# Optimization experiments

Hardware: AMD Instinct MI355X
Metric: run time of the kernel (lower is better)

## Reference

```python
import jax, jax.numpy as jnp
import numpy as np
from jax import lax

# GlobalSeed with a standard Mamba2 (SSD) core.
# C=64 feature channels, G=8 token dim, d_inner=16, d_state=16, nheads=2, headdim=8, d_conv=3.
C_FEAT, G, D_INNER, D_STATE, NHEADS, HEADDIM, D_CONV = 64, 8, 16, 16, 2, 8, 3
CONV_DIM = D_INNER + 2 * D_STATE  # 48
D_IN_PROJ = 2 * D_INNER + 2 * D_STATE + NHEADS  # 66


def setup_inputs() -> dict:
    key = jax.random.key(0)
    ks = jax.random.split(key, 16)
    B, H, W = 16, 128, 128
    s = 0.02
    return {
        "x": jax.random.normal(ks[0], (B, C_FEAT, H, W), jnp.float32),
        "tok_w": s * jax.random.normal(ks[1], (G, C_FEAT), jnp.float32),
        "tok_b": jnp.zeros((G,), jnp.float32),
        "detok_w": s * jax.random.normal(ks[2], (C_FEAT, G), jnp.float32),
        "detok_b": jnp.zeros((C_FEAT,), jnp.float32),
        "in_proj_w": s * jax.random.normal(ks[3], (D_IN_PROJ, G), jnp.float32),
        "in_proj_b": jnp.zeros((D_IN_PROJ,), jnp.float32),
        "conv_w": s * jax.random.normal(ks[4], (CONV_DIM, D_CONV), jnp.float32),
        "conv_b": jnp.zeros((CONV_DIM,), jnp.float32),
        "A_log": jnp.log(jnp.arange(1, NHEADS + 1, dtype=jnp.float32)),
        "D": jnp.ones((NHEADS,), jnp.float32),
        "dt_bias": 0.1 * jax.random.normal(ks[5], (NHEADS,), jnp.float32),
        "norm_w": jnp.ones((D_INNER,), jnp.float32),
        "out_w": s * jax.random.normal(ks[6], (G, D_INNER), jnp.float32),
        "out_b": jnp.zeros((G,), jnp.float32),
    }


def _mamba2(gt, in_proj_w, in_proj_b, conv_w, conv_b, A_log, D, dt_bias, norm_w, out_w, out_b):
    # gt: (B, L, G) tokens
    B, L, _ = gt.shape
    zxbcdt = gt @ in_proj_w.T + in_proj_b  # (B, L, 66)
    z = zxbcdt[..., :D_INNER]
    xBC = zxbcdt[..., D_INNER:D_INNER + CONV_DIM]
    dt = zxbcdt[..., D_INNER + CONV_DIM:]  # (B, L, nheads)
    # depthwise causal conv1d over L
    xBC = lax.conv_general_dilated(
        xBC.transpose(0, 2, 1), conv_w[:, None, :], (1,), [(D_CONV - 1, 0)],
        feature_group_count=CONV_DIM).transpose(0, 2, 1) + conv_b
    xBC = jax.nn.silu(xBC)
    xr = xBC[..., :D_INNER].reshape(B, L, NHEADS, HEADDIM)
    Bm = xBC[..., D_INNER:D_INNER + D_STATE]   # (B, L, N)
    Cm = xBC[..., D_INNER + D_STATE:]          # (B, L, N)
    dt = jax.nn.softplus(dt + dt_bias)          # (B, L, H)
    dec = jnp.exp(dt * (-jnp.exp(A_log)))       # (B, L, H)

    def step(h, inp):
        xt, Bt, Ct, dtt, dct = inp  # (B,H,P) (B,N) (B,N) (B,H) (B,H)
        h = dct[:, :, None, None] * h + (dtt[:, :, None] * xt)[..., None] * Bt[:, None, None, :]
        y = jnp.einsum('bhpn,bn->bhp', h, Ct)
        return h, y

    h0 = jnp.zeros((B, NHEADS, HEADDIM, D_STATE), gt.dtype)
    xs = (xr.transpose(1, 0, 2, 3), Bm.transpose(1, 0, 2), Cm.transpose(1, 0, 2),
          dt.transpose(1, 0, 2), dec.transpose(1, 0, 2))
    _, ys = lax.scan(step, h0, xs)  # (L, B, H, P)
    y = ys.transpose(1, 0, 2, 3) + D[None, None, :, None] * xr
    y = y.reshape(B, L, D_INNER)
    y = y * jax.nn.silu(z)  # gated
    y = y * lax.rsqrt(jnp.mean(y * y, axis=-1, keepdims=True) + 1e-5) * norm_w  # RMSNormGated
    return y @ out_w.T + out_b  # (B, L, G)


def reference(x, tok_w, tok_b, detok_w, detok_b, in_proj_w, in_proj_b, conv_w, conv_b,
              A_log, D, dt_bias, norm_w, out_w, out_b):
    B, C, H, W = x.shape
    L = H * W
    g = jnp.einsum('bchw,gc->bghw', x, tok_w) + tok_b[None, :, None, None]
    gt = g.reshape(B, G, L).transpose(0, 2, 1)  # (B, L, G)
    gt = _mamba2(gt, in_proj_w, in_proj_b, conv_w, conv_b, A_log, D, dt_bias, norm_w, out_w, out_b) + gt
    g2 = gt.transpose(0, 2, 1).reshape(B, G, H, W)
    return x + jnp.einsum('bghw,cg->bchw', g2, detok_w) + detok_b[None, :, None, None]
```

## Files before the change

kernel.cpp:

```cpp
#include <hip/hip_runtime.h>
#include <math.h>

#define NB 16
#define CF 64
#define LL 16384
#define GG 8
#define NH 2
#define SEG 64
#define NSEG 256
#define GRP 16
#define NGRP 16
#define CHK 16
#define NCHKS 4

static constexpr size_t OFF_GT = 0;
static constexpr size_t OFF_C  = OFF_GT + (size_t)NB*LL*GG;
static constexpr size_t OFF_YL = OFF_C  + (size_t)NB*LL*16;
static constexpr size_t OFF_CA = OFF_YL + (size_t)NB*LL*16;
static constexpr size_t OFF_PH = OFF_CA + (size_t)NB*LL*NH;
static constexpr size_t OFF_CP = OFF_PH + (size_t)NB*NSEG*256;
static constexpr size_t OFF_U2 = OFF_CP + (size_t)NB*NSEG*NH;
static constexpr size_t OFF_AG = OFF_U2 + (size_t)NB*NGRP*256;
static constexpr size_t OFF_GH = OFF_AG + (size_t)NB*NGRP*NH;
static constexpr size_t OFF_G2 = OFF_GH + (size_t)NB*NGRP*256;
static constexpr size_t WS_FLOATS = OFF_G2 + (size_t)NB*LL*GG;

__device__ __forceinline__ float siluf(float v){ return v / (1.f + __expf(-v)); }
__device__ __forceinline__ float softplusf(float v){ return v > 20.f ? v : log1pf(__expf(v)); }

__device__ __forceinline__ void load8(float* d, const float* p){
    float4 a = ((const float4*)p)[0];
    float4 b = ((const float4*)p)[1];
    d[0]=a.x; d[1]=a.y; d[2]=a.z; d[3]=a.w;
    d[4]=b.x; d[5]=b.y; d[6]=b.z; d[7]=b.w;
}
__device__ __forceinline__ void load16(float* d, const float* p){
    load8(d, p); load8(d+8, p+8);
}

__global__ __launch_bounds__(256) void k1a_tok(
    const float* __restrict__ x, const float* __restrict__ tok_w,
    const float* __restrict__ tok_b, float* __restrict__ gtw)
{
    __shared__ float s_tok[GG*CF];
    int tid = threadIdx.x;
    int b  = blockIdx.x >> 4;
    int ck = blockIdx.x & 15;
    int l0 = (ck << 10) + (tid << 2);
    for (int i = tid; i < GG*CF; i += 256) s_tok[i] = tok_w[i];
    __syncthreads();
    float acc[4][GG];
    #pragma unroll
    for (int r = 0; r < 4; ++r)
        #pragma unroll
        for (int g = 0; g < GG; ++g) acc[r][g] = tok_b[g];
    const float* xb = x + (size_t)b*CF*LL + l0;
    #pragma unroll 8
    for (int c = 0; c < CF; ++c) {
        float4 xv = *(const float4*)(xb + (size_t)c*LL);
        float xa[4] = {xv.x, xv.y, xv.z, xv.w};
        #pragma unroll
        for (int g = 0; g < GG; ++g) {
            float w = s_tok[g*CF + c];
            #pragma unroll
            for (int r = 0; r < 4; ++r) acc[r][g] = fmaf(xa[r], w, acc[r][g]);
        }
    }
    float* gp = gtw + ((size_t)b*LL + l0)*GG;
    #pragma unroll
    for (int r = 0; r < 4; ++r) {
        ((float4*)gp)[r*2+0] = make_float4(acc[r][0],acc[r][1],acc[r][2],acc[r][3]);
        ((float4*)gp)[r*2+1] = make_float4(acc[r][4],acc[r][5],acc[r][6],acc[r][7]);
    }
}

__global__ __launch_bounds__(256, 1) void k2_fused(
    const float* __restrict__ gtw,
    const float* __restrict__ ipw, const float* __restrict__ ipb,
    const float* __restrict__ cw, const float* __restrict__ cb,
    const float* __restrict__ A_log, const float* __restrict__ dt_bias,
    const float* __restrict__ Dv,
    float* __restrict__ cmw, float* __restrict__ ylw, float* __restrict__ caw,
    float* __restrict__ phw, float* __restrict__ cpw,
    float* __restrict__ U2w, float* __restrict__ Agw)
{
    __shared__ float s_x [16][17][20];
    __shared__ float s_B [16][17][20];
    __shared__ float s_Ct[16][17][20];
    __shared__ float s_dt[16][17][2], s_de[16][17][2], s_ca[16][17][2];
    __shared__ float s_U[16][2][8][17];
    __shared__ float s_cAs[16][2];
    __shared__ float s_ipw[48*8];
    __shared__ float s_ipb2[48], s_cw2[144], s_cb2[48], s_wdt[16];

    int tid = threadIdx.x;
    int b = blockIdx.x >> 4, grp = blockIdx.x & 15;
    for (int i = tid; i < 384; i += 256) s_ipw[i] = ipw[128 + i];
    if (tid < 48) { s_ipb2[tid] = ipb[16 + tid]; s_cb2[tid] = cb[tid]; }
    else if (tid >= 64 && tid < 208) s_cw2[tid - 64] = cw[tid - 64];
    else if (tid >= 224 && tid < 240) s_wdt[tid - 224] = ipw[512 + (tid - 224)];
    __syncthreads();

    int sj = tid >> 4, tl = tid & 15;
    int he = (tid >> 3) & 1, p = tid & 7;
    int hp = he * 8 + p;
    int eb = he * 128 + p * 16;
    float a0e = __expf(A_log[0]), a1e = __expf(A_log[1]);
    float dtb0 = dt_bias[0], dtb1 = dt_bias[1];
    float bdt0 = ipb[64], bdt1 = ipb[65];
    float D_he = Dv[he];
    float h[16];
    #pragma unroll
    for (int n = 0; n < 16; ++n) h[n] = 0.f;
    float cA = 1.f;
    int lb = grp * 1024 + sj * 64;

    for (int c = 0; c < NCHKS; ++c) {
        int l = lb + c * CHK + tl;
        size_t gb = ((size_t)b * LL + l) * GG;
        float g0[8], g1[8], g2v[8];
        #pragma unroll
        for (int g = 0; g < 8; ++g) { g1[g] = 0.f; g2v[g] = 0.f; }
        load8(g0, gtw + gb);
        if (l >= 1) load8(g1, gtw + gb - GG);
        if (l >= 2) load8(g2v, gtw + gb - 2*GG);
        float vals[48];
        #pragma unroll
        for (int ch = 0; ch < 48; ++ch) {
            float4 w0 = *(const float4*)&s_ipw[ch*8];
            float4 w1 = *(const float4*)&s_ipw[ch*8+4];
            float wv[8] = {w0.x,w0.y,w0.z,w0.w,w1.x,w1.y,w1.z,w1.w};
            float bia = s_ipb2[ch];
            float tA = bia, tB = bia, tC = bia;
            #pragma unroll
            for (int g = 0; g < 8; ++g) {
                tA = fmaf(g0[g],  wv[g], tA);
                tB = fmaf(g1[g],  wv[g], tB);
                tC = fmaf(g2v[g], wv[g], tC);
            }
            if (l < 1) tB = 0.f;
            if (l < 2) tC = 0.f;
            float a = s_cb2[ch];
            a = fmaf(tC, s_cw2[ch*3+0], a);
            a = fmaf(tB, s_cw2[ch*3+1], a);
            a = fmaf(tA, s_cw2[ch*3+2], a);
            vals[ch] = siluf(a);
        }
        #pragma unroll
        for (int q = 0; q < 4; ++q) {
            int ph_ = ((q + tl) & 3) * 4;
            *(float4*)&s_x [sj][tl][ph_] = make_float4(vals[q*4+0],vals[q*4+1],vals[q*4+2],vals[q*4+3]);
            *(float4*)&s_B [sj][tl][ph_] = make_float4(vals[16+q*4+0],vals[16+q*4+1],vals[16+q*4+2],vals[16+q*4+3]);
            *(float4*)&s_Ct[sj][tl][ph_] = make_float4(vals[32+q*4+0],vals[32+q*4+1],vals[32+q*4+2],vals[32+q*4+3]);
        }
        {
            size_t pb = (size_t)b * LL + l;
            float4* cp4 = (float4*)(cmw + pb*16);
            #pragma unroll
            for (int q = 0; q < 4; ++q)
                cp4[q] = make_float4(vals[32+q*4+0],vals[32+q*4+1],vals[32+q*4+2],vals[32+q*4+3]);
        }
        {
            float d0 = bdt0, d1 = bdt1;
            #pragma unroll
            for (int g = 0; g < 8; ++g) {
                d0 = fmaf(g0[g], s_wdt[g],   d0);
                d1 = fmaf(g0[g], s_wdt[8+g], d1);
            }
            float dt0 = softplusf(d0 + dtb0), dt1 = softplusf(d1 + dtb1);
            *(float2*)&s_dt[sj][tl][0] = make_float2(dt0, dt1);
            *(float2*)&s_de[sj][tl][0] = make_float2(__expf(-dt0*a0e), __expf(-dt1*a1e));
        }
        __syncthreads();
        for (int t = 0; t < CHK; ++t) {
            float a   = s_de[sj][t][he];
            float dtv = s_dt[sj][t][he];
            float xv  = s_x[sj][t][(((hp>>2)+t)&3)*4 + (hp&3)];
            float u = dtv * xv;
            float Bv[16], Cv[16];
            #pragma unroll
            for (int q = 0; q < 4; ++q) {
                float4 bq = *(const float4*)&s_B [sj][t][((q+t)&3)*4];
                float4 cq = *(const float4*)&s_Ct[sj][t][((q+t)&3)*4];
                Bv[q*4+0]=bq.x; Bv[q*4+1]=bq.y; Bv[q*4+2]=bq.z; Bv[q*4+3]=bq.w;
                Cv[q*4+0]=cq.x; Cv[q*4+1]=cq.y; Cv[q*4+2]=cq.z; Cv[q*4+3]=cq.w;
            }
            float y = 0.f;
            #pragma unroll
            for (int n = 0; n < 16; ++n) {
                h[n] = fmaf(a, h[n], u * Bv[n]);
                y = fmaf(h[n], Cv[n], y);
            }
            cA *= a;
            s_x[sj][t][(((hp>>2)+t)&3)*4 + (hp&3)] = fmaf(D_he, xv, y);
            if (p == 0) s_ca[sj][t][he] = cA;
        }
        __syncthreads();
        {
            size_t pb = (size_t)b * LL + l;
            float4* yp4 = (float4*)(ylw + pb*16);
            #pragma unroll
            for (int q = 0; q < 4; ++q)
                yp4[q] = *(const float4*)&s_x[sj][tl][((q+tl)&3)*4];
            *(float2*)(caw + pb*2) = *(const float2*)&s_ca[sj][tl][0];
        }
        __syncthreads();
    }

    #pragma unroll
    for (int n = 0; n < 16; ++n) s_U[sj][he][p][n] = h[n];
    if (p == 0) s_cAs[sj][he] = cA;
    __syncthreads();
    float hin[16];
    #pragma unroll
    for (int n = 0; n < 16; ++n) hin[n] = 0.f;
    float cp = 1.f;
    for (int j = 0; j < GRP-1; ++j) {
        if (j < sj) {
            float Aj = s_cAs[j][he];
            #pragma unroll
            for (int n = 0; n < 16; ++n) hin[n] = fmaf(Aj, hin[n], s_U[j][he][p][n]);
            cp *= Aj;
        }
    }
    int seg = grp * GRP + sj;
    {
        float* php = phw + (((size_t)b*NSEG + seg) << 8) + eb;
        #pragma unroll
        for (int q = 0; q < 4; ++q)
            ((float4*)php)[q] = make_float4(hin[q*4+0],hin[q*4+1],hin[q*4+2],hin[q*4+3]);
        if (p == 0) cpw[((size_t)b*NSEG + seg)*2 + he] = cp;
    }
    if (sj == GRP-1) {
        float A15 = s_cAs[15][he];
        float* u2p = U2w + (((size_t)b*NGRP + grp) << 8) + eb;
        #pragma unroll
        for (int q = 0; q < 4; ++q) {
            float4 v4;
            v4.x = fmaf(A15, hin[q*4+0], h[q*4+0]);
            v4.y = fmaf(A15, hin[q*4+1], h[q*4+1]);
            v4.z = fmaf(A15, hin[q*4+2], h[q*4+2]);
            v4.w = fmaf(A15, hin[q*4+3], h[q*4+3]);
            ((float4*)u2p)[q] = v4;
        }
        if (p == 0) Agw[((size_t)b*NGRP + grp)*2 + he] = cp * A15;
    }
}

__global__ void k4b_grp(const float* __restrict__ U2w, const float* __restrict__ Agw,
                        float* __restrict__ ghw)
{
    int b = blockIdx.x, e = threadIdx.x, he = e >> 7;
    float u[NGRP], ag[NGRP];
    #pragma unroll
    for (int g = 0; g < NGRP; ++g) {
        u[g]  = U2w[(((size_t)b*NGRP + g) << 8) + e];
        ag[g] = Agw[((size_t)b*NGRP + g)*2 + he];
    }
    float h = 0.f;
    #pragma unroll
    for (int g = 0; g < NGRP; ++g) {
        ghw[(((size_t)b*NGRP + g) << 8) + e] = h;
        h = fmaf(ag[g], h, u[g]);
    }
}

__global__ __launch_bounds__(256, 4) void k5a_epi(
    const float* __restrict__ gtw, const float* __restrict__ cmw,
    const float* __restrict__ ylw, const float* __restrict__ caw,
    const float* __restrict__ phw, const float* __restrict__ cpw,
    const float* __restrict__ ghw,
    const float* __restrict__ ipw, const float* __restrict__ ipb,
    const float* __restrict__ norm_w,
    const float* __restrict__ out_w, const float* __restrict__ out_b,
    float* __restrict__ g2w)
{
    __shared__ float s_hin[4][256];
    __shared__ float s_zw[16*GG], s_ow[GG*16];
    int tid = threadIdx.x;
    int b  = blockIdx.x >> 6;
    int ck = blockIdx.x & 63;
    int grp = ck >> 2;
    float gh = ghw[(((size_t)b*NGRP + grp) << 8) + tid];
    #pragma unroll
    for (int k = 0; k < 4; ++k) {
        int seg = ck*4 + k;
        float cpv = cpw[((size_t)b*NSEG + seg)*2 + (tid >> 7)];
        s_hin[k][tid] = fmaf(cpv, gh, phw[(((size_t)b*NSEG + seg) << 8) + tid]);
    }
    if (tid < 128) s_zw[tid] = ipw[tid];
    else s_ow[tid-128] = out_w[tid-128];
    __syncthreads();
    size_t pb = (size_t)b*LL + (ck<<8) + tid;
    int sub = tid >> 6;
    float gv[8]; load8(gv, gtw + pb*GG);
    float Cv[16], ylv[16];
    load16(Cv,  cmw + pb*16);
    load16(ylv, ylw + pb*16);
    float2 ca = *(const float2*)(caw + pb*2);
    float vv[16], ss = 0.f;
    #pragma unroll
    for (int hp = 0; hp < 16; ++hp) {
        float dot = 0.f;
        #pragma unroll
        for (int nn = 0; nn < 16; ++nn)
            dot = fmaf(Cv[nn], s_hin[sub][(hp>>3)*128 + (hp&7)*16 + nn], dot);
        float zz = ipb[hp];
        #pragma unroll
        for (int g = 0; g < GG; ++g) zz = fmaf(gv[g], s_zw[hp*GG+g], zz);
        float y = fmaf((hp>>3) ? ca.y : ca.x, dot, ylv[hp]);
        float w = y * siluf(zz);
        vv[hp] = w; ss = fmaf(w, w, ss);
    }
    float rn = rsqrtf(ss*(1.f/16.f) + 1e-5f);
    float o[8];
    #pragma unroll
    for (int g = 0; g < GG; ++g) o[g] = out_b[g] + gv[g];
    #pragma unroll
    for (int hp = 0; hp < 16; ++hp) {
        float wv = vv[hp] * rn * norm_w[hp];
        #pragma unroll
        for (int g = 0; g < GG; ++g) o[g] = fmaf(wv, s_ow[g*16+hp], o[g]);
    }
    float* gp = g2w + pb*GG;
    ((float4*)gp)[0] = make_float4(o[0],o[1],o[2],o[3]);
    ((float4*)gp)[1] = make_float4(o[4],o[5],o[6],o[7]);
}

__global__ __launch_bounds__(256, 4) void k5b_detok(
    const float* __restrict__ x, const float* __restrict__ g2w,
    const float* __restrict__ dkw, const float* __restrict__ dkb,
    float* __restrict__ outp)
{
    __shared__ float s_dw[CF*GG];
    __shared__ float s_db[CF];
    int tid = threadIdx.x;
    int b  = blockIdx.x >> 4;
    int ck = blockIdx.x & 15;
    int l0 = (ck << 10) + (tid << 2);
    for (int i = tid; i < CF*GG; i += 256) s_dw[i] = dkw[i];
    if (tid < CF) s_db[tid] = dkb[tid];
    __syncthreads();
    float g2v[4][8];
    const float* gp = g2w + ((size_t)b*LL + l0)*GG;
    #pragma unroll
    for (int r = 0; r < 4; ++r) load8(g2v[r], gp + r*GG);
    const float* xb = x + (size_t)b*CF*LL + l0;
    float* ob = outp + (size_t)b*CF*LL + l0;
    #pragma unroll 4
    for (int c = 0; c < CF; ++c) {
        float4 xv = *(const float4*)(xb + (size_t)c*LL);
        float bias = s_db[c];
        float oa[4] = {xv.x+bias, xv.y+bias, xv.z+bias, xv.w+bias};
        #pragma unroll
        for (int g = 0; g < GG; ++g) {
            float w = s_dw[c*GG+g];
            #pragma unroll
            for (int r = 0; r < 4; ++r) oa[r] = fmaf(g2v[r][g], w, oa[r]);
        }
        *(float4*)(ob + (size_t)c*LL) = make_float4(oa[0],oa[1],oa[2],oa[3]);
    }
}

extern "C" void kernel_launch(void* const* d_in, const int* in_sizes, int n_in,
                              void* d_out, int out_size, void* d_ws, size_t ws_size,
                              hipStream_t stream) {
    const float* x       = (const float*)d_in[0];
    const float* tok_w   = (const float*)d_in[1];
    const float* tok_b   = (const float*)d_in[2];
    const float* detok_w = (const float*)d_in[3];
    const float* detok_b = (const float*)d_in[4];
    const float* ipw     = (const float*)d_in[5];
    const float* ipb     = (const float*)d_in[6];
    const float* cw      = (const float*)d_in[7];
    const float* cb      = (const float*)d_in[8];
    const float* A_log   = (const float*)d_in[9];
    const float* Dv      = (const float*)d_in[10];
    const float* dt_bias = (const float*)d_in[11];
    const float* norm_w  = (const float*)d_in[12];
    const float* out_w   = (const float*)d_in[13];
    const float* out_b   = (const float*)d_in[14];
    float* ws = (float*)d_ws;
    float* outp = (float*)d_out;

    if (ws_size < WS_FLOATS * sizeof(float)) return;

    k1a_tok<<<NB*16, 256, 0, stream>>>(x, tok_w, tok_b, ws+OFF_GT);
    k2_fused<<<NB*NGRP, 256, 0, stream>>>(ws+OFF_GT, ipw, ipb, cw, cb,
        A_log, dt_bias, Dv, ws+OFF_C, ws+OFF_YL, ws+OFF_CA,
        ws+OFF_PH, ws+OFF_CP, ws+OFF_U2, ws+OFF_AG);
    k4b_grp<<<NB, 256, 0, stream>>>(ws+OFF_U2, ws+OFF_AG, ws+OFF_GH);
    k5a_epi<<<NB*64, 256, 0, stream>>>(ws+OFF_GT, ws+OFF_C, ws+OFF_YL, ws+OFF_CA,
        ws+OFF_PH, ws+OFF_CP, ws+OFF_GH, ipw, ipb, norm_w, out_w, out_b, ws+OFF_G2);
    k5b_detok<<<NB*16, 256, 0, stream>>>(x, ws+OFF_G2, detok_w, detok_b, outp);
}
```

Measured before the change: 114.8 us.

## Halve scan segment length, double blocks, and software-pipeline the SSD recurrence

Result: faster. 110.1 us (-4.1%).

```diff
diff --git a/kernel.cpp b/kernel.cpp
--- a/kernel.cpp
+++ b/kernel.cpp
@@ -6,12 +6,12 @@
 #define LL 16384
 #define GG 8
 #define NH 2
-#define SEG 64
-#define NSEG 256
+#define SEG 32
+#define NSEG 512
 #define GRP 16
-#define NGRP 16
+#define NGRP 32
 #define CHK 16
-#define NCHKS 4
+#define NCHKS 2
 
 static constexpr size_t OFF_GT = 0;
 static constexpr size_t OFF_C  = OFF_GT + (size_t)NB*LL*GG;
@@ -74,7 +74,7 @@
     }
 }
 
-__global__ __launch_bounds__(256, 1) void k2_fused(
+__global__ __launch_bounds__(256, 2) void k2_fused(
     const float* __restrict__ gtw,
     const float* __restrict__ ipw, const float* __restrict__ ipb,
     const float* __restrict__ cw, const float* __restrict__ cb,
@@ -87,14 +87,13 @@
     __shared__ float s_x [16][17][20];
     __shared__ float s_B [16][17][20];
     __shared__ float s_Ct[16][17][20];
-    __shared__ float s_dt[16][17][2], s_de[16][17][2], s_ca[16][17][2];
-    __shared__ float s_U[16][2][8][17];
+    __shared__ float s_dt[16][16][2], s_de[16][16][2], s_ca[16][16][2];
     __shared__ float s_cAs[16][2];
     __shared__ float s_ipw[48*8];
     __shared__ float s_ipb2[48], s_cw2[144], s_cb2[48], s_wdt[16];
 
     int tid = threadIdx.x;
-    int b = blockIdx.x >> 4, grp = blockIdx.x & 15;
+    int b = blockIdx.x >> 5, grp = blockIdx.x & 31;
     for (int i = tid; i < 384; i += 256) s_ipw[i] = ipw[128 + i];
     if (tid < 48) { s_ipb2[tid] = ipb[16 + tid]; s_cb2[tid] = cb[tid]; }
     else if (tid >= 64 && tid < 208) s_cw2[tid - 64] = cw[tid - 64];
@@ -113,17 +112,21 @@
     #pragma unroll
     for (int n = 0; n < 16; ++n) h[n] = 0.f;
     float cA = 1.f;
-    int lb = grp * 1024 + sj * 64;
-
-    for (int c = 0; c < NCHKS; ++c) {
-        int l = lb + c * CHK + tl;
+    int lb = grp * (GRP*SEG) + sj * SEG;
+
+    float g0[8], g1[8], g2v[8];
+    {
+        int l = lb + tl;
         size_t gb = ((size_t)b * LL + l) * GG;
-        float g0[8], g1[8], g2v[8];
         #pragma unroll
         for (int g = 0; g < 8; ++g) { g1[g] = 0.f; g2v[g] = 0.f; }
         load8(g0, gtw + gb);
         if (l >= 1) load8(g1, gtw + gb - GG);
         if (l >= 2) load8(g2v, gtw + gb - 2*GG);
+    }
+
+    for (int c = 0; c < NCHKS; ++c) {
+        int l = lb + c * CHK + tl;
         float vals[48];
         #pragma unroll
         for (int ch = 0; ch < 48; ++ch) {
@@ -171,29 +174,59 @@
             *(float2*)&s_dt[sj][tl][0] = make_float2(dt0, dt1);
             *(float2*)&s_de[sj][tl][0] = make_float2(__expf(-dt0*a0e), __expf(-dt1*a1e));
         }
+        if (c + 1 < NCHKS) {
+            int l2 = lb + (c+1) * CHK + tl;
+            size_t gb2 = ((size_t)b * LL + l2) * GG;
+            load8(g0,  gtw + gb2);
+            load8(g1,  gtw + gb2 - GG);
+            load8(g2v, gtw + gb2 - 2*GG);
+        }
         __syncthreads();
-        for (int t = 0; t < CHK; ++t) {
-            float a   = s_de[sj][t][he];
-            float dtv = s_dt[sj][t][he];
-            float xv  = s_x[sj][t][(((hp>>2)+t)&3)*4 + (hp&3)];
-            float u = dtv * xv;
-            float Bv[16], Cv[16];
+        {
+            float a_c  = s_de[sj][0][he];
+            float dt_c = s_dt[sj][0][he];
+            float x_c  = s_x[sj][0][(((hp>>2))&3)*4 + (hp&3)];
+            float4 bq[4], cq[4];
             #pragma unroll
             for (int q = 0; q < 4; ++q) {
-                float4 bq = *(const float4*)&s_B [sj][t][((q+t)&3)*4];
-                float4 cq = *(const float4*)&s_Ct[sj][t][((q+t)&3)*4];
-                Bv[q*4+0]=bq.x; Bv[q*4+1]=bq.y; Bv[q*4+2]=bq.z; Bv[q*4+3]=bq.w;
-                Cv[q*4+0]=cq.x; Cv[q*4+1]=cq.y; Cv[q*4+2]=cq.z; Cv[q*4+3]=cq.w;
+                bq[q] = *(const float4*)&s_B [sj][0][(q&3)*4];
+                cq[q] = *(const float4*)&s_Ct[sj][0][(q&3)*4];
             }
-            float y = 0.f;
-            #pragma unroll
-            for (int n = 0; n < 16; ++n) {
-                h[n] = fmaf(a, h[n], u * Bv[n]);
-                y = fmaf(h[n], Cv[n], y);
+            #pragma unroll
+            for (int t = 0; t < CHK; ++t) {
+                float a = a_c, dtv = dt_c, xv = x_c;
+                float4 nb[4], nc[4];
+                float na = 0.f, ndt = 0.f, nx = 0.f;
+                if (t + 1 < CHK) {
+                    na  = s_de[sj][t+1][he];
+                    ndt = s_dt[sj][t+1][he];
+                    nx  = s_x[sj][t+1][(((hp>>2)+t+1)&3)*4 + (hp&3)];
+                    #pragma unroll
+                    for (int q = 0; q < 4; ++q) {
+                        nb[q] = *(const float4*)&s_B [sj][t+1][((q+t+1)&3)*4];
+                        nc[q] = *(const float4*)&s_Ct[sj][t+1][((q+t+1)&3)*4];
+                    }
+                }
+                float u = dtv * xv;
+                float Bv[16], Cv[16];
+                #pragma unroll
+                for (int q = 0; q < 4; ++q) {
+                    Bv[q*4+0]=bq[q].x; Bv[q*4+1]=bq[q].y; Bv[q*4+2]=bq[q].z; Bv[q*4+3]=bq[q].w;
+                    Cv[q*4+0]=cq[q].x; Cv[q*4+1]=cq[q].y; Cv[q*4+2]=cq[q].z; Cv[q*4+3]=cq[q].w;
+                }
+                float y = 0.f;
+                #pragma unroll
+                for (int n = 0; n < 16; ++n) {
+                    h[n] = fmaf(a, h[n], u * Bv[n]);
+                    y = fmaf(h[n], Cv[n], y);
+                }
+                cA *= a;
+                s_x[sj][t][(((hp>>2)+t)&3)*4 + (hp&3)] = fmaf(D_he, xv, y);
+                if (p == 0) s_ca[sj][t][he] = cA;
+                a_c = na; dt_c = ndt; x_c = nx;
+                #pragma unroll
+                for (int q = 0; q < 4; ++q) { bq[q] = nb[q]; cq[q] = nc[q]; }
             }
-            cA *= a;
-            s_x[sj][t][(((hp>>2)+t)&3)*4 + (hp&3)] = fmaf(D_he, xv, y);
-            if (p == 0) s_ca[sj][t][he] = cA;
         }
         __syncthreads();
         {
@@ -207,6 +240,7 @@
         __syncthreads();
     }
 
+    float (*s_U)[2][8][17] = reinterpret_cast<float(*)[2][8][17]>(&s_x[0][0][0]);
     #pragma unroll
     for (int n = 0; n < 16; ++n) s_U[sj][he][p][n] = h[n];
     if (p == 0) s_cAs[sj][he] = cA;
@@ -275,16 +309,16 @@
     const float* __restrict__ out_w, const float* __restrict__ out_b,
     float* __restrict__ g2w)
 {
-    __shared__ float s_hin[4][256];
+    __shared__ float s_hin[8][256];
     __shared__ float s_zw[16*GG], s_ow[GG*16];
     int tid = threadIdx.x;
     int b  = blockIdx.x >> 6;
     int ck = blockIdx.x & 63;
-    int grp = ck >> 2;
+    int grp = ck >> 1;
     float gh = ghw[(((size_t)b*NGRP + grp) << 8) + tid];
     #pragma unroll
-    for (int k = 0; k < 4; ++k) {
-        int seg = ck*4 + k;
+    for (int k = 0; k < 8; ++k) {
+        int seg = ck*8 + k;
         float cpv = cpw[((size_t)b*NSEG + seg)*2 + (tid >> 7)];
         s_hin[k][tid] = fmaf(cpv, gh, phw[(((size_t)b*NSEG + seg) << 8) + tid]);
     }
@@ -292,7 +326,7 @@
     else s_ow[tid-128] = out_w[tid-128];
     __syncthreads();
     size_t pb = (size_t)b*LL + (ck<<8) + tid;
-    int sub = tid >> 6;
+    int sub = tid >> 5;
     float gv[8]; load8(gv, gtw + pb*GG);
     float Cv[16], ylv[16];
     load16(Cv,  cmw + pb*16);
```

## Replace sequential intra-chunk SSM scan with chunked SSD matmul form

Applied to the files above, without the earlier changes.

Result: slower. 144.7 us (+26.0%).

```diff
diff --git a/kernel.cpp b/kernel.cpp
--- a/kernel.cpp
+++ b/kernel.cpp
@@ -6,21 +6,20 @@
 #define LL 16384
 #define GG 8
 #define NH 2
-#define SEG 64
-#define NSEG 256
-#define GRP 16
+#define CHN 64
+#define NCH 256
 #define NGRP 16
-#define CHK 16
-#define NCHKS 4
 
 static constexpr size_t OFF_GT = 0;
 static constexpr size_t OFF_C  = OFF_GT + (size_t)NB*LL*GG;
 static constexpr size_t OFF_YL = OFF_C  + (size_t)NB*LL*16;
 static constexpr size_t OFF_CA = OFF_YL + (size_t)NB*LL*16;
-static constexpr size_t OFF_PH = OFF_CA + (size_t)NB*LL*NH;
-static constexpr size_t OFF_CP = OFF_PH + (size_t)NB*NSEG*256;
-static constexpr size_t OFF_U2 = OFF_CP + (size_t)NB*NSEG*NH;
-static constexpr size_t OFF_AG = OFF_U2 + (size_t)NB*NGRP*256;
+static constexpr size_t OFF_U2 = OFF_CA + (size_t)NB*LL*NH;
+static constexpr size_t OFF_AC = OFF_U2 + (size_t)NB*NCH*256;
+static constexpr size_t OFF_PH = OFF_AC + (size_t)NB*NCH*NH;
+static constexpr size_t OFF_CP = OFF_PH + (size_t)NB*NCH*256;
+static constexpr size_t OFF_UG = OFF_CP + (size_t)NB*NCH*NH;
+static constexpr size_t OFF_AG = OFF_UG + (size_t)NB*NGRP*256;
 static constexpr size_t OFF_GH = OFF_AG + (size_t)NB*NGRP*NH;
 static constexpr size_t OFF_G2 = OFF_GH + (size_t)NB*NGRP*256;
 static constexpr size_t WS_FLOATS = OFF_G2 + (size_t)NB*LL*GG;
@@ -74,69 +73,56 @@
     }
 }
 
-__global__ __launch_bounds__(256, 1) void k2_fused(
+__global__ __launch_bounds__(256, 4) void k2_ssd(
     const float* __restrict__ gtw,
     const float* __restrict__ ipw, const float* __restrict__ ipb,
     const float* __restrict__ cw, const float* __restrict__ cb,
     const float* __restrict__ A_log, const float* __restrict__ dt_bias,
     const float* __restrict__ Dv,
     float* __restrict__ cmw, float* __restrict__ ylw, float* __restrict__ caw,
-    float* __restrict__ phw, float* __restrict__ cpw,
-    float* __restrict__ U2w, float* __restrict__ Agw)
-{
-    __shared__ float s_x [16][17][20];
-    __shared__ float s_B [16][17][20];
-    __shared__ float s_Ct[16][17][20];
-    __shared__ float s_dt[16][17][2], s_de[16][17][2], s_ca[16][17][2];
-    __shared__ float s_U[16][2][8][17];
-    __shared__ float s_cAs[16][2];
-    __shared__ float s_ipw[48*8];
-    __shared__ float s_ipb2[48], s_cw2[144], s_cb2[48], s_wdt[16];
+    float* __restrict__ U2w, float* __restrict__ Acw)
+{
+    __shared__ float s_x [64][20];
+    __shared__ float s_Ct[64][17];
+    __shared__ float s_BT[16][68];
+    __shared__ float s_G [64][68];
+    __shared__ float s_dt[64][2], s_nda[64][2], s_la[64][2], s_w[64][2];
+    __shared__ float s_ipw[48*8], s_ipb2[48], s_cw2[144], s_cb2[48], s_wdt[16];
 
     int tid = threadIdx.x;
-    int b = blockIdx.x >> 4, grp = blockIdx.x & 15;
+    int b = blockIdx.x >> 8, c = blockIdx.x & 255;
     for (int i = tid; i < 384; i += 256) s_ipw[i] = ipw[128 + i];
     if (tid < 48) { s_ipb2[tid] = ipb[16 + tid]; s_cb2[tid] = cb[tid]; }
     else if (tid >= 64 && tid < 208) s_cw2[tid - 64] = cw[tid - 64];
     else if (tid >= 224 && tid < 240) s_wdt[tid - 224] = ipw[512 + (tid - 224)];
     __syncthreads();
 
-    int sj = tid >> 4, tl = tid & 15;
-    int he = (tid >> 3) & 1, p = tid & 7;
-    int hp = he * 8 + p;
-    int eb = he * 128 + p * 16;
     float a0e = __expf(A_log[0]), a1e = __expf(A_log[1]);
     float dtb0 = dt_bias[0], dtb1 = dt_bias[1];
     float bdt0 = ipb[64], bdt1 = ipb[65];
-    float D_he = Dv[he];
-    float h[16];
-    #pragma unroll
-    for (int n = 0; n < 16; ++n) h[n] = 0.f;
-    float cA = 1.f;
-    int lb = grp * 1024 + sj * 64;
-
-    for (int c = 0; c < NCHKS; ++c) {
-        int l = lb + c * CHK + tl;
-        size_t gb = ((size_t)b * LL + l) * GG;
+    float D0 = Dv[0], D1 = Dv[1];
+
+    {
+        int r = tid >> 2, sub = tid & 3;
+        int l = c*CHN + r;
+        size_t gb = ((size_t)b*LL + l)*GG;
         float g0[8], g1[8], g2v[8];
         #pragma unroll
         for (int g = 0; g < 8; ++g) { g1[g] = 0.f; g2v[g] = 0.f; }
         load8(g0, gtw + gb);
         if (l >= 1) load8(g1, gtw + gb - GG);
         if (l >= 2) load8(g2v, gtw + gb - 2*GG);
-        float vals[48];
-        #pragma unroll
-        for (int ch = 0; ch < 48; ++ch) {
-            float4 w0 = *(const float4*)&s_ipw[ch*8];
-            float4 w1 = *(const float4*)&s_ipw[ch*8+4];
-            float wv[8] = {w0.x,w0.y,w0.z,w0.w,w1.x,w1.y,w1.z,w1.w};
+        #pragma unroll
+        for (int k = 0; k < 12; ++k) {
+            int ch = sub*12 + k;
             float bia = s_ipb2[ch];
             float tA = bia, tB = bia, tC = bia;
             #pragma unroll
             for (int g = 0; g < 8; ++g) {
-                tA = fmaf(g0[g],  wv[g], tA);
-                tB = fmaf(g1[g],  wv[g], tB);
-                tC = fmaf(g2v[g], wv[g], tC);
+                float wv = s_ipw[ch*8+g];
+                tA = fmaf(g0[g],  wv, tA);
+                tB = fmaf(g1[g],  wv, tB);
+                tC = fmaf(g2v[g], wv, tC);
             }
             if (l < 1) tB = 0.f;
             if (l < 2) tC = 0.f;
@@ -144,23 +130,12 @@
             a = fmaf(tC, s_cw2[ch*3+0], a);
             a = fmaf(tB, s_cw2[ch*3+1], a);
             a = fmaf(tA, s_cw2[ch*3+2], a);
-            vals[ch] = siluf(a);
-        }
-        #pragma unroll
-        for (int q = 0; q < 4; ++q) {
-            int ph_ = ((q + tl) & 3) * 4;
-            *(float4*)&s_x [sj][tl][ph_] = make_float4(vals[q*4+0],vals[q*4+1],vals[q*4+2],vals[q*4+3]);
-            *(float4*)&s_B [sj][tl][ph_] = make_float4(vals[16+q*4+0],vals[16+q*4+1],vals[16+q*4+2],vals[16+q*4+3]);
-            *(float4*)&s_Ct[sj][tl][ph_] = make_float4(vals[32+q*4+0],vals[32+q*4+1],vals[32+q*4+2],vals[32+q*4+3]);
-        }
-        {
-            size_t pb = (size_t)b * LL + l;
-            float4* cp4 = (float4*)(cmw + pb*16);
-            #pragma unroll
-            for (int q = 0; q < 4; ++q)
-                cp4[q] = make_float4(vals[32+q*4+0],vals[32+q*4+1],vals[32+q*4+2],vals[32+q*4+3]);
-        }
-        {
+            float v = siluf(a);
+            if (ch < 16)      s_x[r][ch] = v;
+            else if (ch < 32) s_BT[ch-16][r] = v;
+            else              s_Ct[r][ch-32] = v;
+        }
+        if (sub == 0) {
             float d0 = bdt0, d1 = bdt1;
             #pragma unroll
             for (int g = 0; g < 8; ++g) {
@@ -168,100 +143,122 @@
                 d1 = fmaf(g0[g], s_wdt[8+g], d1);
             }
             float dt0 = softplusf(d0 + dtb0), dt1 = softplusf(d1 + dtb1);
-            *(float2*)&s_dt[sj][tl][0] = make_float2(dt0, dt1);
-            *(float2*)&s_de[sj][tl][0] = make_float2(__expf(-dt0*a0e), __expf(-dt1*a1e));
-        }
-        __syncthreads();
-        for (int t = 0; t < CHK; ++t) {
-            float a   = s_de[sj][t][he];
-            float dtv = s_dt[sj][t][he];
-            float xv  = s_x[sj][t][(((hp>>2)+t)&3)*4 + (hp&3)];
-            float u = dtv * xv;
-            float Bv[16], Cv[16];
-            #pragma unroll
-            for (int q = 0; q < 4; ++q) {
-                float4 bq = *(const float4*)&s_B [sj][t][((q+t)&3)*4];
-                float4 cq = *(const float4*)&s_Ct[sj][t][((q+t)&3)*4];
-                Bv[q*4+0]=bq.x; Bv[q*4+1]=bq.y; Bv[q*4+2]=bq.z; Bv[q*4+3]=bq.w;
-                Cv[q*4+0]=cq.x; Cv[q*4+1]=cq.y; Cv[q*4+2]=cq.z; Cv[q*4+3]=cq.w;
+            s_dt[r][0] = dt0; s_dt[r][1] = dt1;
+            s_nda[r][0] = -dt0*a0e; s_nda[r][1] = -dt1*a1e;
+        }
+    }
+    __syncthreads();
+    {
+        int rr = tid >> 2, q = tid & 3;
+        float4 cv = make_float4(s_Ct[rr][q*4+0], s_Ct[rr][q*4+1],
+                                s_Ct[rr][q*4+2], s_Ct[rr][q*4+3]);
+        ((float4*)(cmw + ((size_t)b*LL + c*CHN + rr)*16))[q] = cv;
+    }
+    if (tid < 64) {
+        int rr = tid;
+        float v0 = s_nda[rr][0], v1 = s_nda[rr][1];
+        #pragma unroll
+        for (int off = 1; off < 64; off <<= 1) {
+            float t0 = __shfl_up(v0, off);
+            float t1 = __shfl_up(v1, off);
+            if (rr >= off) { v0 += t0; v1 += t1; }
+        }
+        s_la[rr][0] = v0; s_la[rr][1] = v1;
+        *(float2*)(caw + ((size_t)b*LL + c*CHN + rr)*2) =
+            make_float2(__expf(v0), __expf(v1));
+        float f0 = __shfl(v0, 63), f1 = __shfl(v1, 63);
+        s_w[rr][0] = __expf(f0 - v0) * s_dt[rr][0];
+        s_w[rr][1] = __expf(f1 - v1) * s_dt[rr][1];
+        if (rr == 63)
+            *(float2*)(Acw + ((size_t)b*NCH + c)*2) = make_float2(__expf(f0), __expf(f1));
+    }
+    __syncthreads();
+    {
+        int t0 = (tid >> 4) * 4, s0 = (tid & 15) * 4;
+        float acc[4][4];
+        #pragma unroll
+        for (int i = 0; i < 4; ++i)
+            #pragma unroll
+            for (int j = 0; j < 4; ++j) acc[i][j] = 0.f;
+        #pragma unroll
+        for (int n = 0; n < 16; ++n) {
+            float c0 = s_Ct[t0+0][n], c1 = s_Ct[t0+1][n];
+            float c2 = s_Ct[t0+2][n], c3 = s_Ct[t0+3][n];
+            float4 bb = *(const float4*)&s_BT[n][s0];
+            float bv[4] = {bb.x, bb.y, bb.z, bb.w};
+            #pragma unroll
+            for (int j = 0; j < 4; ++j) {
+                acc[0][j] = fmaf(c0, bv[j], acc[0][j]);
+                acc[1][j] = fmaf(c1, bv[j], acc[1][j]);
+                acc[2][j] = fmaf(c2, bv[j], acc[2][j]);
+                acc[3][j] = fmaf(c3, bv[j], acc[3][j]);
             }
-            float y = 0.f;
-            #pragma unroll
-            for (int n = 0; n < 16; ++n) {
-                h[n] = fmaf(a, h[n], u * Bv[n]);
-                y = fmaf(h[n], Cv[n], y);
-            }
-            cA *= a;
-            s_x[sj][t][(((hp>>2)+t)&3)*4 + (hp&3)] = fmaf(D_he, xv, y);
-            if (p == 0) s_ca[sj][t][he] = cA;
-        }
-        __syncthreads();
-        {
-            size_t pb = (size_t)b * LL + l;
-            float4* yp4 = (float4*)(ylw + pb*16);
-            #pragma unroll
-            for (int q = 0; q < 4; ++q)
-                yp4[q] = *(const float4*)&s_x[sj][tl][((q+tl)&3)*4];
-            *(float2*)(caw + pb*2) = *(const float2*)&s_ca[sj][tl][0];
-        }
-        __syncthreads();
-    }
-
-    #pragma unroll
-    for (int n = 0; n < 16; ++n) s_U[sj][he][p][n] = h[n];
-    if (p == 0) s_cAs[sj][he] = cA;
-    __syncthreads();
-    float hin[16];
-    #pragma unroll
-    for (int n = 0; n < 16; ++n) hin[n] = 0.f;
-    float cp = 1.f;
-    for (int j = 0; j < GRP-1; ++j) {
-        if (j < sj) {
-            float Aj = s_cAs[j][he];
-            #pragma unroll
-            for (int n = 0; n < 16; ++n) hin[n] = fmaf(Aj, hin[n], s_U[j][he][p][n]);
-            cp *= Aj;
-        }
-    }
-    int seg = grp * GRP + sj;
-    {
-        float* php = phw + (((size_t)b*NSEG + seg) << 8) + eb;
-        #pragma unroll
-        for (int q = 0; q < 4; ++q)
-            ((float4*)php)[q] = make_float4(hin[q*4+0],hin[q*4+1],hin[q*4+2],hin[q*4+3]);
-        if (p == 0) cpw[((size_t)b*NSEG + seg)*2 + he] = cp;
-    }
-    if (sj == GRP-1) {
-        float A15 = s_cAs[15][he];
-        float* u2p = U2w + (((size_t)b*NGRP + grp) << 8) + eb;
-        #pragma unroll
-        for (int q = 0; q < 4; ++q) {
-            float4 v4;
-            v4.x = fmaf(A15, hin[q*4+0], h[q*4+0]);
-            v4.y = fmaf(A15, hin[q*4+1], h[q*4+1]);
-            v4.z = fmaf(A15, hin[q*4+2], h[q*4+2]);
-            v4.w = fmaf(A15, hin[q*4+3], h[q*4+3]);
-            ((float4*)u2p)[q] = v4;
-        }
-        if (p == 0) Agw[((size_t)b*NGRP + grp)*2 + he] = cp * A15;
-    }
-}
-
-__global__ void k4b_grp(const float* __restrict__ U2w, const float* __restrict__ Agw,
-                        float* __restrict__ ghw)
+        }
+        #pragma unroll
+        for (int i = 0; i < 4; ++i)
+            *(float4*)&s_G[t0+i][s0] = make_float4(acc[i][0],acc[i][1],acc[i][2],acc[i][3]);
+    }
+    __syncthreads();
+    {
+        int t = tid >> 2, hq = tid & 3, hh = hq >> 1;
+        int pbase = hq * 4;
+        float lat = s_la[t][hh];
+        float Dh = hh ? D1 : D0;
+        float4 xt = *(const float4*)&s_x[t][pbase];
+        float4 acc;
+        acc.x = Dh*xt.x; acc.y = Dh*xt.y; acc.z = Dh*xt.z; acc.w = Dh*xt.w;
+        int send = ((tid >> 6) << 4) + 15;
+        for (int s = 0; s <= send; ++s) {
+            float e = __expf(lat - s_la[s][hh]);
+            float m = (s <= t) ? e * s_G[t][s] * s_dt[s][hh] : 0.f;
+            float4 xs = *(const float4*)&s_x[s][pbase];
+            acc.x = fmaf(m, xs.x, acc.x);
+            acc.y = fmaf(m, xs.y, acc.y);
+            acc.z = fmaf(m, xs.z, acc.z);
+            acc.w = fmaf(m, xs.w, acc.w);
+        }
+        ((float4*)(ylw + ((size_t)b*LL + c*CHN)*16))[tid] = acc;
+    }
+    {
+        int he = tid >> 7, pp = (tid >> 4) & 7, n = tid & 15;
+        float hsum = 0.f;
+        #pragma unroll 8
+        for (int s = 0; s < 64; ++s)
+            hsum = fmaf(s_w[s][he] * s_x[s][he*8+pp], s_BT[n][s], hsum);
+        U2w[(((size_t)b*NCH + c) << 8) + tid] = hsum;
+    }
+}
+
+__global__ void k4c1(const float* __restrict__ U2w, const float* __restrict__ Acw,
+                     float* __restrict__ phw, float* __restrict__ cpw,
+                     float* __restrict__ Ugw, float* __restrict__ Agw)
+{
+    int b = blockIdx.x >> 4, grp = blockIdx.x & 15;
+    int e = threadIdx.x, he = e >> 7;
+    float h = 0.f, cp = 1.f;
+    #pragma unroll
+    for (int j = 0; j < 16; ++j) {
+        int ch = grp*16 + j;
+        size_t ui = (((size_t)b*NCH + ch) << 8) + e;
+        phw[ui] = h;
+        if ((e & 127) == 0) cpw[((size_t)b*NCH + ch)*2 + he] = cp;
+        float A = Acw[((size_t)b*NCH + ch)*2 + he];
+        h = fmaf(A, h, U2w[ui]);
+        cp *= A;
+    }
+    Ugw[(((size_t)b*NGRP + grp) << 8) + e] = h;
+    if ((e & 127) == 0) Agw[((size_t)b*NGRP + grp)*2 + he] = cp;
+}
+
+__global__ void k4c2(const float* __restrict__ Ugw, const float* __restrict__ Agw,
+                     float* __restrict__ ghw)
 {
     int b = blockIdx.x, e = threadIdx.x, he = e >> 7;
-    float u[NGRP], ag[NGRP];
-    #pragma unroll
-    for (int g = 0; g < NGRP; ++g) {
-        u[g]  = U2w[(((size_t)b*NGRP + g) << 8) + e];
-        ag[g] = Agw[((size_t)b*NGRP + g)*2 + he];
-    }
     float h = 0.f;
     #pragma unroll
-    for (int g = 0; g < NGRP; ++g) {
+    for (int g = 0; g < 16; ++g) {
         ghw[(((size_t)b*NGRP + g) << 8) + e] = h;
-        h = fmaf(ag[g], h, u[g]);
+        h = fmaf(Agw[((size_t)b*NGRP + g)*2 + he], h, Ugw[(((size_t)b*NGRP + g) << 8) + e]);
     }
 }
 
@@ -280,13 +277,13 @@
     int tid = threadIdx.x;
     int b  = blockIdx.x >> 6;
     int ck = blockIdx.x & 63;
-    int grp = ck >> 2;
-    float gh = ghw[(((size_t)b*NGRP + grp) << 8) + tid];
+    int grpg = ck >> 2;
+    float gh = ghw[(((size_t)b*NGRP + grpg) << 8) + tid];
     #pragma unroll
     for (int k = 0; k < 4; ++k) {
-        int seg = ck*4 + k;
-        float cpv = cpw[((size_t)b*NSEG + seg)*2 + (tid >> 7)];
-        s_hin[k][tid] = fmaf(cpv, gh, phw[(((size_t)b*NSEG + seg) << 8) + tid]);
+        int chn = ck*4 + k;
+        float cpv = cpw[((size_t)b*NCH + chn)*2 + (tid >> 7)];
+        s_hin[k][tid] = fmaf(cpv, gh, phw[(((size_t)b*NCH + chn) << 8) + tid]);
     }
     if (tid < 128) s_zw[tid] = ipw[tid];
     else s_ow[tid-128] = out_w[tid-128];
@@ -386,10 +383,11 @@
     if (ws_size < WS_FLOATS * sizeof(float)) return;
 
     k1a_tok<<<NB*16, 256, 0, stream>>>(x, tok_w, tok_b, ws+OFF_GT);
-    k2_fused<<<NB*NGRP, 256, 0, stream>>>(ws+OFF_GT, ipw, ipb, cw, cb,
-        A_log, dt_bias, Dv, ws+OFF_C, ws+OFF_YL, ws+OFF_CA,
-        ws+OFF_PH, ws+OFF_CP, ws+OFF_U2, ws+OFF_AG);
-    k4b_grp<<<NB, 256, 0, stream>>>(ws+OFF_U2, ws+OFF_AG, ws+OFF_GH);
+    k2_ssd<<<NB*NCH, 256, 0, stream>>>(ws+OFF_GT, ipw, ipb, cw, cb,
+        A_log, dt_bias, Dv, ws+OFF_C, ws+OFF_YL, ws+OFF_CA, ws+OFF_U2, ws+OFF_AC);
+    k4c1<<<NB*NGRP, 256, 0, stream>>>(ws+OFF_U2, ws+OFF_AC,
+        ws+OFF_PH, ws+OFF_CP, ws+OFF_UG, ws+OFF_AG);
+    k4c2<<<NB, 256, 0, stream>>>(ws+OFF_UG, ws+OFF_AG, ws+OFF_GH);
     k5a_epi<<<NB*64, 256, 0, stream>>>(ws+OFF_GT, ws+OFF_C, ws+OFF_YL, ws+OFF_CA,
         ws+OFF_PH, ws+OFF_CP, ws+OFF_GH, ipw, ipb, norm_w, out_w, out_b, ws+OFF_G2);
     k5b_detok<<<NB*16, 256, 0, stream>>>(x, ws+OFF_G2, detok_w, detok_b, outp);
```
